# Performance work log

Hardware: AMD Instinct MI355X
Metric: run time of the kernel (lower is better)

## Reference

```python
import jax, jax.numpy as jnp
import numpy as np

DX = 0.1  # grid spacing (init arg dx); dy == dx
NX = 4096
NY = 4096


def _pad_bc(X, left, right, top, bottom):
    # X: [1, 1, Nx, Ny]; pad last axis with left/right values, then second-to-last with top/bottom.
    B, C, Nx, Ny = X.shape
    l = jnp.broadcast_to(left, (B, C, Nx, 1)).astype(X.dtype)
    r = jnp.broadcast_to(right, (B, C, Nx, 1)).astype(X.dtype)
    X = jnp.concatenate([l, X, r], axis=3)
    t = jnp.broadcast_to(top, (B, C, 1, Ny + 2)).astype(X.dtype)
    bo = jnp.broadcast_to(bottom, (B, C, 1, Ny + 2)).astype(X.dtype)
    return jnp.concatenate([t, X, bo], axis=2)


def _laplacian(Xp):
    # 5-point stencil, equivalent to conv2d with [[0,1,0],[1,-4,1],[0,1,0]]/dx^2 (valid padding).
    inv_dx2 = 1.0 / (DX * DX)
    return (
        Xp[:, :, :-2, 1:-1]
        + Xp[:, :, 2:, 1:-1]
        + Xp[:, :, 1:-1, :-2]
        + Xp[:, :, 1:-1, 2:]
        - 4.0 * Xp[:, :, 1:-1, 1:-1]
    ) * inv_dx2


def setup_inputs() -> dict:
    key = jax.random.key(0)
    k1, k2 = jax.random.split(key)
    state = jax.random.normal(k1, (1, 2, NX, NY), dtype=jnp.float32)
    bc = jax.random.uniform(k2, (1, 2, 4), dtype=jnp.float32)
    a_org = jnp.asarray(-2.0, dtype=jnp.float32)
    b_org = jnp.asarray(-2.0, dtype=jnp.float32)
    k_org = jnp.asarray(-2.0, dtype=jnp.float32)
    return {"state": state, "bc": bc, "a_org": a_org, "b_org": b_org, "k_org": k_org}


def reference(state, bc, a_org, b_org, k_org):
    a = jax.nn.sigmoid(a_org) * 0.01
    b = jax.nn.sigmoid(b_org) * 0.01
    k = jax.nn.sigmoid(k_org) * 0.01

    U = state[:, :1]  # [1,1,Nx,Ny]
    V = state[:, 1:]

    U_ = _pad_bc(U, bc[0, 0, 0], bc[0, 0, 1], bc[0, 0, 2], bc[0, 0, 3])
    V_ = _pad_bc(V, bc[0, 1, 0], bc[0, 1, 1], bc[0, 1, 2], bc[0, 1, 3])

    delta_u = _laplacian(U_)
    delta_v = _laplacian(V_)

    dUdt = a * delta_u + U - U ** 3 - V - k
    dVdt = b * delta_v + U - V
    return jnp.concatenate([dUdt, dVdt], axis=1)
```

## Files before the change

kernel.cpp:

```cpp
#include <hip/hip_runtime.h>

#define NXD 4096
#define NYD 4096

__global__ __launch_bounds__(256) void DiffReactParamPDE_85478439125433_kernel(
    const float* __restrict__ state,
    const float* __restrict__ bc,
    const float* __restrict__ a_org,
    const float* __restrict__ b_org,
    const float* __restrict__ k_org,
    float* __restrict__ out)
{
    const float inv_dx2 = 100.0f;

    const float a = 0.01f / (1.0f + expf(-a_org[0]));
    const float b = 0.01f / (1.0f + expf(-b_org[0]));
    const float k = 0.01f / (1.0f + expf(-k_org[0]));

    const float uL = bc[0], uR = bc[1], uT = bc[2], uB = bc[3];
    const float vL = bc[4], vR = bc[5], vT = bc[6], vB = bc[7];

    const int j0 = (blockIdx.x * blockDim.x + threadIdx.x) * 4;
    const int i  = blockIdx.y;
    if (j0 >= NYD || i >= NXD) return;

    const float* __restrict__ U = state;
    const float* __restrict__ V = state + (size_t)NXD * NYD;
    float* __restrict__ dU = out;
    float* __restrict__ dV = out + (size_t)NXD * NYD;

    const size_t base = (size_t)i * NYD + j0;

    const float4 uc = *(const float4*)(U + base);
    const float4 vc = *(const float4*)(V + base);

    float4 uu, ud, vu, vd;
    if (i > 0) {
        uu = *(const float4*)(U + base - NYD);
        vu = *(const float4*)(V + base - NYD);
    } else {
        uu = make_float4(uT, uT, uT, uT);
        vu = make_float4(vT, vT, vT, vT);
    }
    if (i < NXD - 1) {
        ud = *(const float4*)(U + base + NYD);
        vd = *(const float4*)(V + base + NYD);
    } else {
        ud = make_float4(uB, uB, uB, uB);
        vd = make_float4(vB, vB, vB, vB);
    }

    const float ul = (j0 > 0)        ? U[base - 1] : uL;
    const float ur = (j0 + 4 < NYD)  ? U[base + 4] : uR;
    const float vl = (j0 > 0)        ? V[base - 1] : vL;
    const float vr = (j0 + 4 < NYD)  ? V[base + 4] : vR;

    float lu0 = (uu.x + ud.x + ul   + uc.y - 4.0f * uc.x) * inv_dx2;
    float lu1 = (uu.y + ud.y + uc.x + uc.z - 4.0f * uc.y) * inv_dx2;
    float lu2 = (uu.z + ud.z + uc.y + uc.w - 4.0f * uc.z) * inv_dx2;
    float lu3 = (uu.w + ud.w + uc.z + ur   - 4.0f * uc.w) * inv_dx2;

    float lv0 = (vu.x + vd.x + vl   + vc.y - 4.0f * vc.x) * inv_dx2;
    float lv1 = (vu.y + vd.y + vc.x + vc.z - 4.0f * vc.y) * inv_dx2;
    float lv2 = (vu.z + vd.z + vc.y + vc.w - 4.0f * vc.z) * inv_dx2;
    float lv3 = (vu.w + vd.w + vc.z + vr   - 4.0f * vc.w) * inv_dx2;

    float4 du_out;
    du_out.x = a * lu0 + uc.x - uc.x * uc.x * uc.x - vc.x - k;
    du_out.y = a * lu1 + uc.y - uc.y * uc.y * uc.y - vc.y - k;
    du_out.z = a * lu2 + uc.z - uc.z * uc.z * uc.z - vc.z - k;
    du_out.w = a * lu3 + uc.w - uc.w * uc.w * uc.w - vc.w - k;

    float4 dv_out;
    dv_out.x = b * lv0 + uc.x - vc.x;
    dv_out.y = b * lv1 + uc.y - vc.y;
    dv_out.z = b * lv2 + uc.z - vc.z;
    dv_out.w = b * lv3 + uc.w - vc.w;

    *(float4*)(dU + base) = du_out;
    *(float4*)(dV + base) = dv_out;
}

extern "C" void kernel_launch(void* const* d_in, const int* in_sizes, int n_in,
                              void* d_out, int out_size, void* d_ws, size_t ws_size,
                              hipStream_t stream) {
    const float* state = (const float*)d_in[0];
    const float* bc    = (const float*)d_in[1];
    const float* a_org = (const float*)d_in[2];
    const float* b_org = (const float*)d_in[3];
    const float* k_org = (const float*)d_in[4];
    float* out = (float*)d_out;

    dim3 block(256, 1, 1);
    dim3 grid(NYD / (4 * 256), NXD, 1);
    DiffReactParamPDE_85478439125433_kernel<<<grid, block, 0, stream>>>(
        state, bc, a_org, b_org, k_org, out);
}
```

Measured before the change: 247.1 us.

## Process four rows per thread with register reuse and nontemporal stores

```diff
diff --git a/kernel.cpp b/kernel.cpp
--- a/kernel.cpp
+++ b/kernel.cpp
@@ -2,6 +2,9 @@
 
 #define NXD 4096
 #define NYD 4096
+#define ROWS 4
+
+typedef float f32x4 __attribute__((ext_vector_type(4)));
 
 __global__ __launch_bounds__(256) void DiffReactParamPDE_85478439125433_kernel(
     const float* __restrict__ state,
@@ -20,65 +23,74 @@
     const float uL = bc[0], uR = bc[1], uT = bc[2], uB = bc[3];
     const float vL = bc[4], vR = bc[5], vT = bc[6], vB = bc[7];
 
-    const int j0 = (blockIdx.x * blockDim.x + threadIdx.x) * 4;
-    const int i  = blockIdx.y;
-    if (j0 >= NYD || i >= NXD) return;
+    const int j0 = (blockIdx.x * 256 + threadIdx.x) * 4;
+    const int i0 = blockIdx.y * ROWS;
 
     const float* __restrict__ U = state;
     const float* __restrict__ V = state + (size_t)NXD * NYD;
     float* __restrict__ dU = out;
     float* __restrict__ dV = out + (size_t)NXD * NYD;
 
-    const size_t base = (size_t)i * NYD + j0;
+    const size_t rowbase = (size_t)i0 * NYD + j0;
 
-    const float4 uc = *(const float4*)(U + base);
-    const float4 vc = *(const float4*)(V + base);
-
-    float4 uu, ud, vu, vd;
-    if (i > 0) {
-        uu = *(const float4*)(U + base - NYD);
-        vu = *(const float4*)(V + base - NYD);
-    } else {
-        uu = make_float4(uT, uT, uT, uT);
-        vu = make_float4(vT, vT, vT, vT);
-    }
-    if (i < NXD - 1) {
-        ud = *(const float4*)(U + base + NYD);
-        vd = *(const float4*)(V + base + NYD);
-    } else {
-        ud = make_float4(uB, uB, uB, uB);
-        vd = make_float4(vB, vB, vB, vB);
+    float4 u[ROWS + 2], v[ROWS + 2];
+#pragma unroll
+    for (int r = 0; r < ROWS + 2; ++r) {
+        const int row = i0 - 1 + r;
+        if (row >= 0 && row < NXD) {
+            const size_t bofs = (size_t)row * NYD + j0;
+            u[r] = *(const float4*)(U + bofs);
+            v[r] = *(const float4*)(V + bofs);
+        } else if (row < 0) {
+            u[r] = make_float4(uT, uT, uT, uT);
+            v[r] = make_float4(vT, vT, vT, vT);
+        } else {
+            u[r] = make_float4(uB, uB, uB, uB);
+            v[r] = make_float4(vB, vB, vB, vB);
+        }
     }
 
-    const float ul = (j0 > 0)        ? U[base - 1] : uL;
-    const float ur = (j0 + 4 < NYD)  ? U[base + 4] : uR;
-    const float vl = (j0 > 0)        ? V[base - 1] : vL;
-    const float vr = (j0 + 4 < NYD)  ? V[base + 4] : vR;
+    float ulft[ROWS], urgt[ROWS], vlft[ROWS], vrgt[ROWS];
+#pragma unroll
+    for (int r = 0; r < ROWS; ++r) {
+        const size_t bo = rowbase + (size_t)r * NYD;
+        ulft[r] = (j0 > 0)       ? U[bo - 1] : uL;
+        urgt[r] = (j0 + 4 < NYD) ? U[bo + 4] : uR;
+        vlft[r] = (j0 > 0)       ? V[bo - 1] : vL;
+        vrgt[r] = (j0 + 4 < NYD) ? V[bo + 4] : vR;
+    }
 
-    float lu0 = (uu.x + ud.x + ul   + uc.y - 4.0f * uc.x) * inv_dx2;
-    float lu1 = (uu.y + ud.y + uc.x + uc.z - 4.0f * uc.y) * inv_dx2;
-    float lu2 = (uu.z + ud.z + uc.y + uc.w - 4.0f * uc.z) * inv_dx2;
-    float lu3 = (uu.w + ud.w + uc.z + ur   - 4.0f * uc.w) * inv_dx2;
+#pragma unroll
+    for (int r = 0; r < ROWS; ++r) {
+        const float4 cu = u[r + 1], cv = v[r + 1];
+        const float4 au = u[r],     bu = u[r + 2];
+        const float4 av = v[r],     bv = v[r + 2];
 
-    float lv0 = (vu.x + vd.x + vl   + vc.y - 4.0f * vc.x) * inv_dx2;
-    float lv1 = (vu.y + vd.y + vc.x + vc.z - 4.0f * vc.y) * inv_dx2;
-    float lv2 = (vu.z + vd.z + vc.y + vc.w - 4.0f * vc.z) * inv_dx2;
-    float lv3 = (vu.w + vd.w + vc.z + vr   - 4.0f * vc.w) * inv_dx2;
+        const float lu0 = (au.x + bu.x + ulft[r] + cu.y - 4.0f * cu.x) * inv_dx2;
+        const float lu1 = (au.y + bu.y + cu.x    + cu.z - 4.0f * cu.y) * inv_dx2;
+        const float lu2 = (au.z + bu.z + cu.y    + cu.w - 4.0f * cu.z) * inv_dx2;
+        const float lu3 = (au.w + bu.w + cu.z + urgt[r] - 4.0f * cu.w) * inv_dx2;
 
-    float4 du_out;
-    du_out.x = a * lu0 + uc.x - uc.x * uc.x * uc.x - vc.x - k;
-    du_out.y = a * lu1 + uc.y - uc.y * uc.y * uc.y - vc.y - k;
-    du_out.z = a * lu2 + uc.z - uc.z * uc.z * uc.z - vc.z - k;
-    du_out.w = a * lu3 + uc.w - uc.w * uc.w * uc.w - vc.w - k;
+        const float lv0 = (av.x + bv.x + vlft[r] + cv.y - 4.0f * cv.x) * inv_dx2;
+        const float lv1 = (av.y + bv.y + cv.x    + cv.z - 4.0f * cv.y) * inv_dx2;
+        const float lv2 = (av.z + bv.z + cv.y    + cv.w - 4.0f * cv.z) * inv_dx2;
+        const float lv3 = (av.w + bv.w + cv.z + vrgt[r] - 4.0f * cv.w) * inv_dx2;
 
-    float4 dv_out;
-    dv_out.x = b * lv0 + uc.x - vc.x;
-    dv_out.y = b * lv1 + uc.y - vc.y;
-    dv_out.z = b * lv2 + uc.z - vc.z;
-    dv_out.w = b * lv3 + uc.w - vc.w;
+        f32x4 duo, dvo;
+        duo.x = a * lu0 + cu.x - cu.x * cu.x * cu.x - cv.x - k;
+        duo.y = a * lu1 + cu.y - cu.y * cu.y * cu.y - cv.y - k;
+        duo.z = a * lu2 + cu.z - cu.z * cu.z * cu.z - cv.z - k;
+        duo.w = a * lu3 + cu.w - cu.w * cu.w * cu.w - cv.w - k;
 
-    *(float4*)(dU + base) = du_out;
-    *(float4*)(dV + base) = dv_out;
+        dvo.x = b * lv0 + cu.x - cv.x;
+        dvo.y = b * lv1 + cu.y - cv.y;
+        dvo.z = b * lv2 + cu.z - cv.z;
+        dvo.w = b * lv3 + cu.w - cv.w;
+
+        const size_t bo = rowbase + (size_t)r * NYD;
+        __builtin_nontemporal_store(duo, (f32x4*)(dU + bo));
+        __builtin_nontemporal_store(dvo, (f32x4*)(dV + bo));
+    }
 }
 
 extern "C" void kernel_launch(void* const* d_in, const int* in_sizes, int n_in,
@@ -92,7 +104,7 @@
     float* out = (float*)d_out;
 
     dim3 block(256, 1, 1);
-    dim3 grid(NYD / (4 * 256), NXD, 1);
+    dim3 grid(NYD / (4 * 256), NXD / ROWS, 1);
     DiffReactParamPDE_85478439125433_kernel<<<grid, block, 0, stream>>>(
         state, bc, a_org, b_org, k_org, out);
 }
```

New measurement: 250.3 us. About the same (+1.3%).
